# Kernel optimization log

Measured on AMD Instinct MI355X. Metric: run time of the kernel, lower is better.

The kernel has to match this reference:

```python
import jax, jax.numpy as jnp
import numpy as np

H = W = 256
C = 256
N_ROIS = 2000
POOL = 7


def setup_inputs() -> dict:
    key = jax.random.key(0)
    kf, kw, kh, kx, ky = jax.random.split(key, 5)
    feature_map = jax.random.normal(kf, (1, H, W, C), dtype=jnp.float32)
    # ROI format: (batch_idx, x, y, w, h), integer pixel coords, in-bounds
    w = jax.random.randint(kw, (N_ROIS,), 8, 65)
    h = jax.random.randint(kh, (N_ROIS,), 8, 65)
    x = jax.random.randint(kx, (N_ROIS,), 0, W - 64)
    y = jax.random.randint(ky, (N_ROIS,), 0, H - 64)
    rois = jnp.stack([jnp.zeros_like(x), x, y, w, h], axis=1).astype(jnp.int32)
    return {"feature_map": feature_map, "rois": rois, "pool_size": POOL}


def _axis_coords(start, length, pool_size):
    """Sample coords along one axis, matching tf.image.resize bilinear
    (half-pixel centers) applied to the crop [start, start+length).
    start, length: [N] int. Returns abs idx0, idx1 [N,P] int and frac [N,P]."""
    lf = length.astype(jnp.float32)
    # source coord within the crop for each output pixel
    f = (jnp.arange(pool_size, dtype=jnp.float32) + 0.5)[None, :] * (lf / pool_size)[:, None] - 0.5
    f = jnp.clip(f, 0.0, (lf - 1.0)[:, None])
    i0 = jnp.floor(f).astype(jnp.int32)
    i1 = jnp.minimum(i0 + 1, (length - 1)[:, None])
    frac = f - i0.astype(jnp.float32)
    return start[:, None] + i0, start[:, None] + i1, frac


def _roi_pool(feature_map, rois, pool_size):
    fm = feature_map[0]                      # [H, W, C]
    x, y, w, h = rois[:, 1], rois[:, 2], rois[:, 3], rois[:, 4]
    y0, y1, fy = _axis_coords(y, h, pool_size)   # [N, P]
    x0, x1, fx = _axis_coords(x, w, pool_size)   # [N, P]

    def g(yi, xi):  # gather -> [N, P, P, C]
        return fm[yi[:, :, None], xi[:, None, :], :]

    fx_ = fx[:, None, :, None]
    fy_ = fy[:, :, None, None]
    top = g(y0, x0) * (1.0 - fx_) + g(y0, x1) * fx_
    bot = g(y1, x0) * (1.0 - fx_) + g(y1, x1) * fx_
    return top * (1.0 - fy_) + bot * fy_     # [N, P, P, C]


def reference(feature_map, rois, pool_size):
    return _roi_pool(feature_map, rois, pool_size)
```

## Files before the change

### kernel.cpp

```cpp
#include <hip/hip_runtime.h>

#define FH 256
#define FW 256
#define FC 256
#define POOL 7

typedef float f32x4 __attribute__((ext_vector_type(4)));

__global__ __launch_bounds__(256) void roi_pool_kernel(
    const float* __restrict__ fm,
    const int*   __restrict__ rois,
    float*       __restrict__ out,
    int n_cells)
{
    int t    = blockIdx.x * blockDim.x + threadIdx.x;
    int lane = threadIdx.x & 63;
    int cell = __builtin_amdgcn_readfirstlane(t >> 6);
    if (cell >= n_cells) return;

    int pi  = cell % POOL;
    int tmp = cell / POOL;
    int pj  = tmp % POOL;
    int roi = tmp / POOL;

    int rx = rois[roi * 5 + 1];
    int ry = rois[roi * 5 + 2];
    int rw = rois[roi * 5 + 3];
    int rh = rois[roi * 5 + 4];

    float lfh = (float)rh;
    float fy  = ((float)pj + 0.5f) * (lfh / (float)POOL) - 0.5f;
    fy = fminf(fmaxf(fy, 0.0f), lfh - 1.0f);
    int   j0 = (int)floorf(fy);
    int   j1 = min(j0 + 1, rh - 1);
    float wy = fy - (float)j0;
    int   y0 = ry + j0;
    int   y1 = ry + j1;

    float lfw = (float)rw;
    float fx  = ((float)pi + 0.5f) * (lfw / (float)POOL) - 0.5f;
    fx = fminf(fmaxf(fx, 0.0f), lfw - 1.0f);
    int   i0 = (int)floorf(fx);
    int   i1 = min(i0 + 1, rw - 1);
    float wx = fx - (float)i0;
    int   x0 = rx + i0;
    int   x1 = rx + i1;

    const f32x4* p00 = (const f32x4*)(fm + ((size_t)y0 * FW + x0) * FC) + lane;
    const f32x4* p01 = (const f32x4*)(fm + ((size_t)y0 * FW + x1) * FC) + lane;
    const f32x4* p10 = (const f32x4*)(fm + ((size_t)y1 * FW + x0) * FC) + lane;
    const f32x4* p11 = (const f32x4*)(fm + ((size_t)y1 * FW + x1) * FC) + lane;

    f32x4 a = *p00;
    f32x4 b = *p01;
    f32x4 c = *p10;
    f32x4 d = *p11;

    float owx = 1.0f - wx;
    float owy = 1.0f - wy;

    f32x4 r = (a * owx + b * wx) * owy + (c * owx + d * wx) * wy;

    f32x4* o = (f32x4*)(out + (size_t)cell * FC) + lane;
    __builtin_nontemporal_store(r, o);
}

extern "C" void kernel_launch(void* const* d_in, const int* in_sizes, int n_in,
                              void* d_out, int out_size, void* d_ws, size_t ws_size,
                              hipStream_t stream) {
    const float* fm   = (const float*)d_in[0];
    const int*   rois = (const int*)d_in[1];
    float* out = (float*)d_out;

    int n_rois  = in_sizes[1] / 5;
    int n_cells = n_rois * POOL * POOL;
    int total   = n_cells * (FC / 4);
    int block   = 256;
    int grid    = (total + block - 1) / block;

    roi_pool_kernel<<<grid, block, 0, stream>>>(fm, rois, out, n_cells);
}
```

Before: 183.9 us.

## Process four cells per wave and remap blocks for XCD-local ROI grouping

Each wave now computes four consecutive output cells, issuing all sixteen gather loads before doing any blending, so more memory requests are in flight per wave. Block indices are also permuted so that consecutive logical blocks, and therefore cells of the same ROI, run on the same XCD and can reuse its L2. The cost is higher register pressure per thread and fewer waves in total, which could reduce latency hiding if occupancy drops.

```diff
diff --git a/kernel.cpp b/kernel.cpp
--- a/kernel.cpp
+++ b/kernel.cpp
@@ -4,6 +4,7 @@
 #define FW 256
 #define FC 256
 #define POOL 7
+#define CPW 4
 
 typedef float f32x4 __attribute__((ext_vector_type(4)));
 
@@ -11,58 +12,65 @@
     const float* __restrict__ fm,
     const int*   __restrict__ rois,
     float*       __restrict__ out,
-    int n_cells)
+    int n_cells, int chunk)
 {
-    int t    = blockIdx.x * blockDim.x + threadIdx.x;
+    int b  = blockIdx.x;
+    int lb = (b & 7) * chunk + (b >> 3);
+
     int lane = threadIdx.x & 63;
-    int cell = __builtin_amdgcn_readfirstlane(t >> 6);
-    if (cell >= n_cells) return;
+    int wave = threadIdx.x >> 6;
+    int base_cell = __builtin_amdgcn_readfirstlane((lb * 4 + wave) * CPW);
+    if (base_cell >= n_cells) return;
 
-    int pi  = cell % POOL;
-    int tmp = cell / POOL;
-    int pj  = tmp % POOL;
-    int roi = tmp / POOL;
+    f32x4 A[CPW], B[CPW], C[CPW], D[CPW];
+    float WX[CPW], WY[CPW];
 
-    int rx = rois[roi * 5 + 1];
-    int ry = rois[roi * 5 + 2];
-    int rw = rois[roi * 5 + 3];
-    int rh = rois[roi * 5 + 4];
+#pragma unroll
+    for (int c = 0; c < CPW; ++c) {
+        int cell = base_cell + c;
+        int pi  = cell % POOL;
+        int tmp = cell / POOL;
+        int pj  = tmp % POOL;
+        int roi = tmp / POOL;
 
-    float lfh = (float)rh;
-    float fy  = ((float)pj + 0.5f) * (lfh / (float)POOL) - 0.5f;
-    fy = fminf(fmaxf(fy, 0.0f), lfh - 1.0f);
-    int   j0 = (int)floorf(fy);
-    int   j1 = min(j0 + 1, rh - 1);
-    float wy = fy - (float)j0;
-    int   y0 = ry + j0;
-    int   y1 = ry + j1;
+        int rx = rois[roi * 5 + 1];
+        int ry = rois[roi * 5 + 2];
+        int rw = rois[roi * 5 + 3];
+        int rh = rois[roi * 5 + 4];
 
-    float lfw = (float)rw;
-    float fx  = ((float)pi + 0.5f) * (lfw / (float)POOL) - 0.5f;
-    fx = fminf(fmaxf(fx, 0.0f), lfw - 1.0f);
-    int   i0 = (int)floorf(fx);
-    int   i1 = min(i0 + 1, rw - 1);
-    float wx = fx - (float)i0;
-    int   x0 = rx + i0;
-    int   x1 = rx + i1;
+        float lfh = (float)rh;
+        float fy  = ((float)pj + 0.5f) * (lfh / (float)POOL) - 0.5f;
+        fy = fminf(fmaxf(fy, 0.0f), lfh - 1.0f);
+        int   j0 = (int)floorf(fy);
+        int   j1 = min(j0 + 1, rh - 1);
+        WY[c] = fy - (float)j0;
+        int   y0 = ry + j0;
+        int   y1 = ry + j1;
 
-    const f32x4* p00 = (const f32x4*)(fm + ((size_t)y0 * FW + x0) * FC) + lane;
-    const f32x4* p01 = (const f32x4*)(fm + ((size_t)y0 * FW + x1) * FC) + lane;
-    const f32x4* p10 = (const f32x4*)(fm + ((size_t)y1 * FW + x0) * FC) + lane;
-    const f32x4* p11 = (const f32x4*)(fm + ((size_t)y1 * FW + x1) * FC) + lane;
+        float lfw = (float)rw;
+        float fx  = ((float)pi + 0.5f) * (lfw / (float)POOL) - 0.5f;
+        fx = fminf(fmaxf(fx, 0.0f), lfw - 1.0f);
+        int   i0 = (int)floorf(fx);
+        int   i1 = min(i0 + 1, rw - 1);
+        WX[c] = fx - (float)i0;
+        int   x0 = rx + i0;
+        int   x1 = rx + i1;
 
-    f32x4 a = *p00;
-    f32x4 b = *p01;
-    f32x4 c = *p10;
-    f32x4 d = *p11;
+        A[c] = *((const f32x4*)(fm + ((size_t)y0 * FW + x0) * FC) + lane);
+        B[c] = *((const f32x4*)(fm + ((size_t)y0 * FW + x1) * FC) + lane);
+        C[c] = *((const f32x4*)(fm + ((size_t)y1 * FW + x0) * FC) + lane);
+        D[c] = *((const f32x4*)(fm + ((size_t)y1 * FW + x1) * FC) + lane);
+    }
 
-    float owx = 1.0f - wx;
-    float owy = 1.0f - wy;
-
-    f32x4 r = (a * owx + b * wx) * owy + (c * owx + d * wx) * wy;
-
-    f32x4* o = (f32x4*)(out + (size_t)cell * FC) + lane;
-    __builtin_nontemporal_store(r, o);
+#pragma unroll
+    for (int c = 0; c < CPW; ++c) {
+        float wx = WX[c], wy = WY[c];
+        float owx = 1.0f - wx, owy = 1.0f - wy;
+        f32x4 r = (A[c] * owx + B[c] * wx) * owy
+                + (C[c] * owx + D[c] * wx) * wy;
+        f32x4* o = (f32x4*)(out + (size_t)(base_cell + c) * FC) + lane;
+        __builtin_nontemporal_store(r, o);
+    }
 }
 
 extern "C" void kernel_launch(void* const* d_in, const int* in_sizes, int n_in,
@@ -74,9 +82,10 @@
 
     int n_rois  = in_sizes[1] / 5;
     int n_cells = n_rois * POOL * POOL;
-    int total   = n_cells * (FC / 4);
-    int block   = 256;
-    int grid    = (total + block - 1) / block;
+    int n_waves = (n_cells + CPW - 1) / CPW;
+    int blocks  = (n_waves + 3) / 4;
+    blocks      = (blocks + 7) & ~7;
+    int chunk   = blocks / 8;
 
-    roi_pool_kernel<<<grid, block, 0, stream>>>(fm, rois, out, n_cells);
+    roi_pool_kernel<<<blocks, 256, 0, stream>>>(fm, rois, out, n_cells, chunk);
 }
```

After: 183.1 us. Within noise of the previous version (-0.4%).
